# Optimization experiments

Hardware: AMD Instinct MI355X
Metric: run time of the kernel (lower is better)

Reference implementation:

```python
import jax, jax.numpy as jnp
import numpy as np

B, T, C = 4, 4096, 1024
DEGREE, EXPAND = 2, 2
H = EXPAND * C  # selector / inner dim = 2048


def setup_inputs() -> dict:
    key = jax.random.key(0)
    ks = jax.random.split(key, 4)
    sc = lambda d: 1.0 / np.sqrt(d)
    return {
        "x": jax.random.normal(ks[0], (B, T, C), jnp.float32),
        "W_sel": jax.random.normal(ks[1], (C, H), jnp.float32) * sc(C),
        "W_agg": jax.random.normal(ks[2], (C, DEGREE * H), jnp.float32) * sc(C),
        "W_out": jax.random.normal(ks[3], (H, C), jnp.float32) * sc(H),
        "sqk_q": jnp.ones((H,), jnp.float32),
        "sqk_k": jnp.ones((DEGREE * H,), jnp.float32),
    }


def reference(x, W_sel, W_agg, W_out, sqk_q, sqk_k):
    # Selector branch on queries (gated): B,T,H
    s = jax.nn.silu(jnp.einsum('btc,ch->bth', x, W_sel) * sqk_q)
    # Aggregator branch on context: B,T,DEGREE*H
    h = jnp.einsum('btc,cd->btd', x, W_agg) * sqk_k
    chunks = jnp.split(h, DEGREE, axis=-1)
    # Polynomial expansion: sum_{d=1..DEGREE} prod_{k<=d} chunk_k  -> B,T,H
    p = chunks[0]
    poly = p
    for c in chunks[1:]:
        p = p * c
        poly = poly + p
    # Causal masked mean: tril(ones(T,T)) @ poly / row-count == cumsum / arange.
    # Honors the causal structure without materializing the T x T mask.
    denom = jnp.arange(1, T + 1, dtype=poly.dtype)[None, :, None]
    agg = jnp.cumsum(poly, axis=1) / denom  # B,T,H causal running mean
    # Mix selected queries with aggregated polynomial state, project out.
    return jnp.einsum('bth,hc->btc', s * agg, W_out)
```

## Files before the change

### kernel.cpp

```cpp
#include <hip/hip_runtime.h>
#include <hip/hip_bf16.h>
#include <stdint.h>

#define BB 4
#define TT 4096
#define CC 1024
#define HH 2048
#define MM (BB*TT)
#define NCK 32
#define CKS 128

using short8 = __attribute__((ext_vector_type(8))) short;
using f32x4  = __attribute__((ext_vector_type(4))) float;

__device__ __forceinline__ unsigned short f2bf(float f) {
    union { float f; uint32_t u; } v; v.f = f;
    uint32_t r = v.u + 0x7fffu + ((v.u >> 16) & 1u);
    return (unsigned short)(r >> 16);
}
__device__ __forceinline__ float bf_lo(uint32_t u) {
    union { uint32_t u; float f; } v; v.u = u << 16; return v.f;
}
__device__ __forceinline__ float bf_hi(uint32_t u) {
    union { uint32_t u; float f; } v; v.u = u & 0xFFFF0000u; return v.f;
}
__device__ __forceinline__ uint32_t pack2bf(float lo, float hi) {
    return ((uint32_t)f2bf(lo)) | (((uint32_t)f2bf(hi)) << 16);
}

__global__ void conv_x_kernel(const float* __restrict__ x, unsigned short* __restrict__ xb, int n4) {
    int i = blockIdx.x * blockDim.x + threadIdx.x;
    if (i >= n4) return;
    float4 v = ((const float4*)x)[i];
    ushort4 o;
    o.x = f2bf(v.x); o.y = f2bf(v.y); o.z = f2bf(v.z); o.w = f2bf(v.w);
    ((ushort4*)xb)[i] = o;
}

__global__ void trans_direct_kernel(const float* __restrict__ in, unsigned short* __restrict__ out,
                                    const float* __restrict__ scale, int R, int Cin) {
    __shared__ float tile[32][33];
    int c0 = blockIdx.x * 32, k0 = blockIdx.y * 32;
    int tx = threadIdx.x;
    for (int i = threadIdx.y; i < 32; i += 8) {
        float s = scale ? scale[c0 + tx] : 1.f;
        tile[i][tx] = in[(size_t)(k0 + i) * Cin + c0 + tx] * s;
    }
    __syncthreads();
    for (int i = threadIdx.y; i < 32; i += 8)
        out[(size_t)(c0 + i) * R + k0 + tx] = f2bf(tile[tx][i]);
}

__global__ void trans_pair_kernel(const float* __restrict__ in, unsigned short* __restrict__ out,
                                  const float* __restrict__ scale) {
    __shared__ float tile[32][33];
    int q0 = blockIdx.x * 32, k0 = blockIdx.y * 32;
    int g = q0 >> 5;
    int tx = threadIdx.x;
    int c = (tx < 16) ? (g * 16 + tx) : (2048 + g * 16 + tx - 16);
    float s = scale[c];
    for (int i = threadIdx.y; i < 32; i += 8)
        tile[i][tx] = in[(size_t)(k0 + i) * 4096 + c] * s;
    __syncthreads();
    for (int i = threadIdx.y; i < 32; i += 8)
        out[(size_t)(q0 + i) * 1024 + k0 + tx] = f2bf(tile[tx][i]);
}

template<int LDK, int NT>
__device__ __forceinline__ void gemm_core(
    const unsigned short* __restrict__ A,
    const unsigned short* __restrict__ Bt,
    int m0, int n0, int tid,
    f32x4 (&acc)[8][4])
{
    __shared__ __align__(16) unsigned short As[4 * 8192];
    __shared__ __align__(16) unsigned short Bs[4 * 8192];

    const int lane = tid & 63;
    const int wave = tid >> 6;
    const int l15  = lane & 15;
    const int quad = lane >> 4;
    const int wm = (wave >> 2) << 7;
    const int wn = (wave & 3) << 6;

#pragma unroll
    for (int i = 0; i < 8; i++)
#pragma unroll
        for (int j = 0; j < 4; j++) acc[i][j] = {0.f, 0.f, 0.f, 0.f};

    const int rl  = tid >> 2;
    const int kc8 = ((tid & 3) ^ ((tid >> 3) & 3)) << 3;
    const unsigned short* gA = A  + (size_t)(m0 + rl) * LDK + kc8;
    const unsigned short* gB = Bt + (size_t)(n0 + rl) * LDK + kc8;

#define STAGE(G, L) __builtin_amdgcn_global_load_lds( \
        (const __attribute__((address_space(1))) void*)(G), \
        (__attribute__((address_space(3))) void*)(L), 16, 0, 0)

#pragma unroll
    for (int t = 0; t < 2; t++) {
        STAGE(gA + t * 32,             &As[t * 8192 + tid * 8]);
        STAGE(gA + 128 * LDK + t * 32, &As[t * 8192 + 4096 + tid * 8]);
        STAGE(gB + t * 32,             &Bs[t * 8192 + tid * 8]);
        STAGE(gB + 128 * LDK + t * 32, &Bs[t * 8192 + 4096 + tid * 8]);
    }
    asm volatile("s_waitcnt vmcnt(4)" ::: "memory");
    __builtin_amdgcn_s_barrier();

    for (int t = 0; t < NT; ++t) {
        const unsigned short* as = &As[(t & 3) * 8192];
        const unsigned short* bs = &Bs[(t & 3) * 8192];
        unsigned short* asd = &As[((t + 2) & 3) * 8192];
        unsigned short* bsd = &Bs[((t + 2) & 3) * 8192];
        const bool pf = (t + 2) < NT;

        short8 af[4], bf[4];
#pragma unroll
        for (int i = 0; i < 4; i++) {
            int row = wm + i * 16 + l15;
            af[i] = *(const short8*)(as + row * 32 + ((quad ^ ((row >> 1) & 3)) << 3));
        }
#pragma unroll
        for (int j = 0; j < 4; j++) {
            int row = wn + j * 16 + l15;
            bf[j] = *(const short8*)(bs + row * 32 + ((quad ^ ((row >> 1) & 3)) << 3));
        }
        if (pf) {
            STAGE(gA + (t + 2) * 32,             asd + tid * 8);
            STAGE(gA + 128 * LDK + (t + 2) * 32, asd + 4096 + tid * 8);
        }
        __builtin_amdgcn_s_barrier();
        asm volatile("s_waitcnt lgkmcnt(0)" ::: "memory");
        __builtin_amdgcn_sched_barrier(0);
        __builtin_amdgcn_s_setprio(1);
#pragma unroll
        for (int i = 0; i < 4; i++)
#pragma unroll
            for (int j = 0; j < 4; j++)
                acc[i][j] = __builtin_amdgcn_mfma_f32_16x16x32_bf16(af[i], bf[j], acc[i][j], 0, 0, 0);
        __builtin_amdgcn_s_setprio(0);
        __builtin_amdgcn_sched_barrier(0);
        __builtin_amdgcn_s_barrier();

        short8 ag[4];
#pragma unroll
        for (int i = 0; i < 4; i++) {
            int row = wm + 64 + i * 16 + l15;
            ag[i] = *(const short8*)(as + row * 32 + ((quad ^ ((row >> 1) & 3)) << 3));
        }
        if (pf) {
            STAGE(gB + (t + 2) * 32,             bsd + tid * 8);
            STAGE(gB + 128 * LDK + (t + 2) * 32, bsd + 4096 + tid * 8);
        }
        __builtin_amdgcn_s_barrier();
        asm volatile("s_waitcnt lgkmcnt(0)" ::: "memory");
        __builtin_amdgcn_sched_barrier(0);
        __builtin_amdgcn_s_setprio(1);
#pragma unroll
        for (int i = 0; i < 4; i++)
#pragma unroll
            for (int j = 0; j < 4; j++)
                acc[4 + i][j] = __builtin_amdgcn_mfma_f32_16x16x32_bf16(ag[i], bf[j], acc[4 + i][j], 0, 0, 0);
        __builtin_amdgcn_s_setprio(0);
        __builtin_amdgcn_sched_barrier(0);
        if (t < NT - 2) { asm volatile("s_waitcnt vmcnt(4)" ::: "memory"); }
        else            { asm volatile("s_waitcnt vmcnt(0)" ::: "memory"); }
        __builtin_amdgcn_s_barrier();
    }
#undef STAGE
}

__global__ __launch_bounds__(512, 2) void gemm_fused_kernel(
    const unsigned short* __restrict__ A,
    const unsigned short* __restrict__ Bt,
    unsigned short* __restrict__ Sout,
    unsigned short* __restrict__ Pout,
    float* __restrict__ part)
{
    __shared__ float psum[256];
    const int tid = threadIdx.x;
    const int mt = blockIdx.x / 24;
    const int nt = blockIdx.x % 24;
    const int m0 = mt << 8, n0 = nt << 8;
    if (tid < 256) psum[tid] = 0.f;

    f32x4 acc[8][4];
    gemm_core<1024, 32>(A, Bt, m0, n0, tid, acc);

    const int lane = tid & 63;
    const int wave = tid >> 6;
    const int l15  = lane & 15;
    const int quad = lane >> 4;
    const int wm = (wave >> 2) << 7;
    const int wn = (wave & 3) << 6;

    if (nt < 8) {
#pragma unroll
        for (int i = 0; i < 8; i++)
#pragma unroll
            for (int j = 0; j < 4; j++) {
                int col = n0 + wn + j * 16 + l15;
#pragma unroll
                for (int r = 0; r < 4; r++) {
                    int row = m0 + wm + i * 16 + quad * 4 + r;
                    float v = acc[i][j][r];
                    v = v / (1.f + __expf(-v));
                    Sout[(size_t)row * 2048 + col] = f2bf(v);
                }
            }
    } else {
        const int pbase = ((n0 - 2048 + wn) >> 1);
        float lsum0 = 0.f, lsum1 = 0.f;
#pragma unroll
        for (int i = 0; i < 8; i++) {
#pragma unroll
            for (int jp = 0; jp < 2; jp++) {
                int pcol = pbase + jp * 16 + l15;
#pragma unroll
                for (int r = 0; r < 4; r++) {
                    int row = m0 + wm + i * 16 + quad * 4 + r;
                    float pv = acc[i][2 * jp][r] * (1.f + acc[i][2 * jp + 1][r]);
                    Pout[(size_t)row * 2048 + pcol] = f2bf(pv);
                    if (jp == 0) lsum0 += pv; else lsum1 += pv;
                }
            }
        }
        int base = (wm >> 7) * 128 + (wn >> 1) + l15;
        atomicAdd(&psum[base], lsum0);
        atomicAdd(&psum[base + 16], lsum1);
        __syncthreads();
        if (tid < 256) {
            int b  = m0 >> 12;
            int ck = ((m0 & 4095) >> 7) + (tid >> 7);
            part[((size_t)b * NCK + ck) * 2048 + ((n0 - 2048) >> 1) + (tid & 127)] = psum[tid];
        }
    }
}

__global__ __launch_bounds__(512, 2) void gemm_out_kernel(
    const unsigned short* __restrict__ A,
    const unsigned short* __restrict__ Bt,
    float* __restrict__ Cout)
{
    const int tid = threadIdx.x;
    const int mt = blockIdx.x >> 2;
    const int nt = blockIdx.x & 3;
    const int m0 = mt << 8, n0 = nt << 8;

    f32x4 acc[8][4];
    gemm_core<2048, 64>(A, Bt, m0, n0, tid, acc);

    const int lane = tid & 63;
    const int wave = tid >> 6;
    const int l15  = lane & 15;
    const int quad = lane >> 4;
    const int wm = (wave >> 2) << 7;
    const int wn = (wave & 3) << 6;
#pragma unroll
    for (int i = 0; i < 8; i++)
#pragma unroll
        for (int j = 0; j < 4; j++) {
            int col = n0 + wn + j * 16 + l15;
#pragma unroll
            for (int r = 0; r < 4; r++) {
                int row = m0 + wm + i * 16 + quad * 4 + r;
                Cout[(size_t)row * 1024 + col] = acc[i][j][r];
            }
        }
}

__global__ void chunk_scan_kernel(float* __restrict__ part) {
    int idx = blockIdx.x * blockDim.x + threadIdx.x;
    int b = idx >> 11, col = idx & 2047;
    float run = 0.f;
    for (int ck = 0; ck < NCK; ck++) {
        size_t off = ((size_t)b * NCK + ck) * 2048 + col;
        float v = part[off];
        part[off] = run;
        run += v;
    }
}

__global__ void finalize_kernel(unsigned short* __restrict__ poly, const unsigned short* __restrict__ s,
                                const float* __restrict__ part) {
    int seg = blockIdx.x & 3;
    int ck  = (blockIdx.x >> 2) & (NCK - 1);
    int b   = blockIdx.x >> 7;
    int cp  = seg * 256 + threadIdx.x;
    size_t po = ((size_t)b * NCK + ck) * 2048 + cp * 2;
    float run0 = part[po], run1 = part[po + 1];
    size_t base = ((size_t)b * TT + (size_t)ck * CKS) * 2048 + cp * 2;
    for (int t = 0; t < CKS; t++) {
        int tg = ck * CKS + t;
        size_t off = base + (size_t)t * 2048;
        uint32_t pv = *(const uint32_t*)&poly[off];
        run0 += bf_lo(pv);
        run1 += bf_hi(pv);
        float inv = 1.f / (float)(tg + 1);
        uint32_t sv = *(const uint32_t*)&s[off];
        float m0 = bf_lo(sv) * run0 * inv;
        float m1 = bf_hi(sv) * run1 * inv;
        *(uint32_t*)&poly[off] = pack2bf(m0, m1);
    }
}

extern "C" void kernel_launch(void* const* d_in, const int* in_sizes, int n_in,
                              void* d_out, int out_size, void* d_ws, size_t ws_size,
                              hipStream_t stream) {
    const float* x     = (const float*)d_in[0];
    const float* W_sel = (const float*)d_in[1];
    const float* W_agg = (const float*)d_in[2];
    const float* W_out = (const float*)d_in[3];
    const float* sqk_q = (const float*)d_in[4];
    const float* sqk_k = (const float*)d_in[5];
    float* out = (float*)d_out;

    char* ws = (char*)d_ws;
    unsigned short* xb    = (unsigned short*)(ws);
    unsigned short* wallT = (unsigned short*)(ws + 33554432ull);
    unsigned short* woutT = (unsigned short*)(ws + 46137344ull);
    unsigned short* s_b   = (unsigned short*)(ws + 50331648ull);
    unsigned short* poly  = (unsigned short*)(ws + 117440512ull);
    float*          part  = (float*)(ws + 184549376ull);

    dim3 tb(32, 8);
    conv_x_kernel<<<(MM * CC / 4 + 255) / 256, 256, 0, stream>>>(x, xb, MM * CC / 4);
    trans_direct_kernel<<<dim3(HH / 32, CC / 32), tb, 0, stream>>>(W_sel, wallT, sqk_q, CC, HH);
    trans_pair_kernel<<<dim3(4096 / 32, CC / 32), tb, 0, stream>>>(W_agg, wallT + 2048ull * 1024, sqk_k);
    trans_direct_kernel<<<dim3(CC / 32, HH / 32), tb, 0, stream>>>(W_out, woutT, nullptr, HH, CC);

    gemm_fused_kernel<<<(MM / 256) * 24, 512, 0, stream>>>(xb, wallT, s_b, poly, part);

    chunk_scan_kernel<<<(BB * HH) / 256, 256, 0, stream>>>(part);
    finalize_kernel<<<BB * NCK * 4, 256, 0, stream>>>(poly, s_b, part);

    gemm_out_kernel<<<(MM / 256) * (CC / 256), 512, 0, stream>>>(poly, woutT, out);
}
```

Before: 473.0 us.

## Double-buffer LDS fragment loads and cut barriers per K-step in GEMM core

Restructures the GEMM main loop so the A/B register fragments for the next K-step are read from LDS while the current step's second MFMA half is still computing, using two register fragment buffers. The loop is unrolled by 4 over the LDS ring so buffer indices are compile-time constants. All four prefetch loads are issued at the start of each step, and the three barriers per step become one. The aim is to hide LDS read latency and remove barrier stalls, at the cost of more VGPRs under a 2-blocks-per-CU launch bound. Partial lgkmcnt waits also add ordering risk.

```diff
diff --git a/kernel.cpp b/kernel.cpp
--- a/kernel.cpp
+++ b/kernel.cpp
@@ -96,78 +96,94 @@
 #define STAGE(G, L) __builtin_amdgcn_global_load_lds( \
         (const __attribute__((address_space(1))) void*)(G), \
         (__attribute__((address_space(3))) void*)(L), 16, 0, 0)
+#define SWZ(row) ((quad ^ (((row) >> 1) & 3)) << 3)
 
 #pragma unroll
     for (int t = 0; t < 2; t++) {
         STAGE(gA + t * 32,             &As[t * 8192 + tid * 8]);
-        STAGE(gA + 128 * LDK + t * 32, &As[t * 8192 + 4096 + tid * 8]);
+        STAGE(gA + 128 * (size_t)LDK + t * 32, &As[t * 8192 + 4096 + tid * 8]);
         STAGE(gB + t * 32,             &Bs[t * 8192 + tid * 8]);
-        STAGE(gB + 128 * LDK + t * 32, &Bs[t * 8192 + 4096 + tid * 8]);
+        STAGE(gB + 128 * (size_t)LDK + t * 32, &Bs[t * 8192 + 4096 + tid * 8]);
     }
     asm volatile("s_waitcnt vmcnt(4)" ::: "memory");
     __builtin_amdgcn_s_barrier();
 
-    for (int t = 0; t < NT; ++t) {
-        const unsigned short* as = &As[(t & 3) * 8192];
-        const unsigned short* bs = &Bs[(t & 3) * 8192];
-        unsigned short* asd = &As[((t + 2) & 3) * 8192];
-        unsigned short* bsd = &Bs[((t + 2) & 3) * 8192];
-        const bool pf = (t + 2) < NT;
-
-        short8 af[4], bf[4];
-#pragma unroll
-        for (int i = 0; i < 4; i++) {
-            int row = wm + i * 16 + l15;
-            af[i] = *(const short8*)(as + row * 32 + ((quad ^ ((row >> 1) & 3)) << 3));
+    short8 afb[2][4], bfb[2][4], ag[4];
+#pragma unroll
+    for (int i = 0; i < 4; i++) {
+        int row = wm + i * 16 + l15;
+        afb[0][i] = *(const short8*)(&As[0] + row * 32 + SWZ(row));
+    }
+#pragma unroll
+    for (int j = 0; j < 4; j++) {
+        int row = wn + j * 16 + l15;
+        bfb[0][j] = *(const short8*)(&Bs[0] + row * 32 + SWZ(row));
+    }
+
+    for (int tb = 0; tb < NT; tb += 4) {
+#pragma unroll
+        for (int u = 0; u < 4; ++u) {
+            const int t   = tb + u;
+            const int cur = u & 1;
+            const int nxt = cur ^ 1;
+            const unsigned short* as  = &As[u * 8192];
+            const unsigned short* asn = &As[((u + 1) & 3) * 8192];
+            const unsigned short* bsn = &Bs[((u + 1) & 3) * 8192];
+            unsigned short* asd = &As[((u + 2) & 3) * 8192];
+            unsigned short* bsd = &Bs[((u + 2) & 3) * 8192];
+
+            if (t + 2 < NT) {
+                STAGE(gA + (size_t)(t + 2) * 32,                       asd + tid * 8);
+                STAGE(gA + 128 * (size_t)LDK + (size_t)(t + 2) * 32,   asd + 4096 + tid * 8);
+                STAGE(gB + (size_t)(t + 2) * 32,                       bsd + tid * 8);
+                STAGE(gB + 128 * (size_t)LDK + (size_t)(t + 2) * 32,   bsd + 4096 + tid * 8);
+            }
+#pragma unroll
+            for (int i = 0; i < 4; i++) {
+                int row = wm + 64 + i * 16 + l15;
+                ag[i] = *(const short8*)(as + row * 32 + SWZ(row));
+            }
+            asm volatile("s_waitcnt lgkmcnt(4)" ::: "memory");
+            __builtin_amdgcn_sched_barrier(0);
+            __builtin_amdgcn_s_setprio(1);
+#pragma unroll
+            for (int i = 0; i < 4; i++)
+#pragma unroll
+                for (int j = 0; j < 4; j++)
+                    acc[i][j] = __builtin_amdgcn_mfma_f32_16x16x32_bf16(afb[cur][i], bfb[cur][j], acc[i][j], 0, 0, 0);
+            __builtin_amdgcn_s_setprio(0);
+            __builtin_amdgcn_sched_barrier(0);
+            if (t < NT - 2) { asm volatile("s_waitcnt vmcnt(4)" ::: "memory"); }
+            else            { asm volatile("s_waitcnt vmcnt(0)" ::: "memory"); }
+            __builtin_amdgcn_s_barrier();
+            if (t + 1 < NT) {
+#pragma unroll
+                for (int i = 0; i < 4; i++) {
+                    int row = wm + i * 16 + l15;
+                    afb[nxt][i] = *(const short8*)(asn + row * 32 + SWZ(row));
+                }
+#pragma unroll
+                for (int j = 0; j < 4; j++) {
+                    int row = wn + j * 16 + l15;
+                    bfb[nxt][j] = *(const short8*)(bsn + row * 32 + SWZ(row));
+                }
+                asm volatile("s_waitcnt lgkmcnt(8)" ::: "memory");
+            } else {
+                asm volatile("s_waitcnt lgkmcnt(0)" ::: "memory");
+            }
+            __builtin_amdgcn_sched_barrier(0);
+            __builtin_amdgcn_s_setprio(1);
+#pragma unroll
+            for (int i = 0; i < 4; i++)
+#pragma unroll
+                for (int j = 0; j < 4; j++)
+                    acc[4 + i][j] = __builtin_amdgcn_mfma_f32_16x16x32_bf16(ag[i], bfb[cur][j], acc[4 + i][j], 0, 0, 0);
+            __builtin_amdgcn_s_setprio(0);
+            __builtin_amdgcn_sched_barrier(0);
         }
-#pragma unroll
-        for (int j = 0; j < 4; j++) {
-            int row = wn + j * 16 + l15;
-            bf[j] = *(const short8*)(bs + row * 32 + ((quad ^ ((row >> 1) & 3)) << 3));
-        }
-        if (pf) {
-            STAGE(gA + (t + 2) * 32,             asd + tid * 8);
-            STAGE(gA + 128 * LDK + (t + 2) * 32, asd + 4096 + tid * 8);
-        }
-        __builtin_amdgcn_s_barrier();
-        asm volatile("s_waitcnt lgkmcnt(0)" ::: "memory");
-        __builtin_amdgcn_sched_barrier(0);
-        __builtin_amdgcn_s_setprio(1);
-#pragma unroll
-        for (int i = 0; i < 4; i++)
-#pragma unroll
-            for (int j = 0; j < 4; j++)
-                acc[i][j] = __builtin_amdgcn_mfma_f32_16x16x32_bf16(af[i], bf[j], acc[i][j], 0, 0, 0);
-        __builtin_amdgcn_s_setprio(0);
-        __builtin_amdgcn_sched_barrier(0);
-        __builtin_amdgcn_s_barrier();
-
-        short8 ag[4];
-#pragma unroll
-        for (int i = 0; i < 4; i++) {
-            int row = wm + 64 + i * 16 + l15;
-            ag[i] = *(const short8*)(as + row * 32 + ((quad ^ ((row >> 1) & 3)) << 3));
-        }
-        if (pf) {
-            STAGE(gB + (t + 2) * 32,             bsd + tid * 8);
-            STAGE(gB + 128 * LDK + (t + 2) * 32, bsd + 4096 + tid * 8);
-        }
-        __builtin_amdgcn_s_barrier();
-        asm volatile("s_waitcnt lgkmcnt(0)" ::: "memory");
-        __builtin_amdgcn_sched_barrier(0);
-        __builtin_amdgcn_s_setprio(1);
-#pragma unroll
-        for (int i = 0; i < 4; i++)
-#pragma unroll
-            for (int j = 0; j < 4; j++)
-                acc[4 + i][j] = __builtin_amdgcn_mfma_f32_16x16x32_bf16(ag[i], bf[j], acc[4 + i][j], 0, 0, 0);
-        __builtin_amdgcn_s_setprio(0);
-        __builtin_amdgcn_sched_barrier(0);
-        if (t < NT - 2) { asm volatile("s_waitcnt vmcnt(4)" ::: "memory"); }
-        else            { asm volatile("s_waitcnt vmcnt(0)" ::: "memory"); }
-        __builtin_amdgcn_s_barrier();
     }
 #undef STAGE
+#undef SWZ
 }
 
 __global__ __launch_bounds__(512, 2) void gemm_fused_kernel(
```

New measurement: 590.5 us. 24.8% more time.

## Software-pipeline LDS fragment loads across k-tiles and drop the per-tile barrier

Applied to the files above, without the earlier changes.

Restructures the GEMM main loop so the next tile's A/B register fragments are read from LDS while the current tile's second MFMA half runs. Fragment sets are double-buffered and the loop is unrolled by 4, cutting the barriers per k-step from three to one. It also removes the min-blocks-per-CU of 2 from launch bounds, which lets the compiler use more registers for the extra fragment buffers, possibly at the cost of occupancy. The single barrier and partial lgkmcnt waits make correctness depend on the exact ordering of LDS reuse across the 4-stage ring.

```diff
diff --git a/kernel.cpp b/kernel.cpp
--- a/kernel.cpp
+++ b/kernel.cpp
@@ -96,81 +96,99 @@
 #define STAGE(G, L) __builtin_amdgcn_global_load_lds( \
         (const __attribute__((address_space(1))) void*)(G), \
         (__attribute__((address_space(3))) void*)(L), 16, 0, 0)
+#define SWZ(row) ((quad ^ (((row) >> 1) & 3)) << 3)
 
 #pragma unroll
     for (int t = 0; t < 2; t++) {
-        STAGE(gA + t * 32,             &As[t * 8192 + tid * 8]);
-        STAGE(gA + 128 * LDK + t * 32, &As[t * 8192 + 4096 + tid * 8]);
-        STAGE(gB + t * 32,             &Bs[t * 8192 + tid * 8]);
-        STAGE(gB + 128 * LDK + t * 32, &Bs[t * 8192 + 4096 + tid * 8]);
+        STAGE(gA + t * 32,                     &As[t * 8192 + tid * 8]);
+        STAGE(gA + 128 * (size_t)LDK + t * 32, &As[t * 8192 + 4096 + tid * 8]);
+        STAGE(gB + t * 32,                     &Bs[t * 8192 + tid * 8]);
+        STAGE(gB + 128 * (size_t)LDK + t * 32, &Bs[t * 8192 + 4096 + tid * 8]);
     }
     asm volatile("s_waitcnt vmcnt(4)" ::: "memory");
     __builtin_amdgcn_s_barrier();
 
-    for (int t = 0; t < NT; ++t) {
-        const unsigned short* as = &As[(t & 3) * 8192];
-        const unsigned short* bs = &Bs[(t & 3) * 8192];
-        unsigned short* asd = &As[((t + 2) & 3) * 8192];
-        unsigned short* bsd = &Bs[((t + 2) & 3) * 8192];
-        const bool pf = (t + 2) < NT;
-
-        short8 af[4], bf[4];
-#pragma unroll
-        for (int i = 0; i < 4; i++) {
-            int row = wm + i * 16 + l15;
-            af[i] = *(const short8*)(as + row * 32 + ((quad ^ ((row >> 1) & 3)) << 3));
-        }
-#pragma unroll
-        for (int j = 0; j < 4; j++) {
-            int row = wn + j * 16 + l15;
-            bf[j] = *(const short8*)(bs + row * 32 + ((quad ^ ((row >> 1) & 3)) << 3));
-        }
-        if (pf) {
-            STAGE(gA + (t + 2) * 32,             asd + tid * 8);
-            STAGE(gA + 128 * LDK + (t + 2) * 32, asd + 4096 + tid * 8);
-        }
-        __builtin_amdgcn_s_barrier();
-        asm volatile("s_waitcnt lgkmcnt(0)" ::: "memory");
-        __builtin_amdgcn_sched_barrier(0);
-        __builtin_amdgcn_s_setprio(1);
-#pragma unroll
-        for (int i = 0; i < 4; i++)
-#pragma unroll
-            for (int j = 0; j < 4; j++)
-                acc[i][j] = __builtin_amdgcn_mfma_f32_16x16x32_bf16(af[i], bf[j], acc[i][j], 0, 0, 0);
-        __builtin_amdgcn_s_setprio(0);
-        __builtin_amdgcn_sched_barrier(0);
-        __builtin_amdgcn_s_barrier();
-
-        short8 ag[4];
-#pragma unroll
-        for (int i = 0; i < 4; i++) {
-            int row = wm + 64 + i * 16 + l15;
-            ag[i] = *(const short8*)(as + row * 32 + ((quad ^ ((row >> 1) & 3)) << 3));
-        }
-        if (pf) {
-            STAGE(gB + (t + 2) * 32,             bsd + tid * 8);
-            STAGE(gB + 128 * LDK + (t + 2) * 32, bsd + 4096 + tid * 8);
-        }
-        __builtin_amdgcn_s_barrier();
-        asm volatile("s_waitcnt lgkmcnt(0)" ::: "memory");
-        __builtin_amdgcn_sched_barrier(0);
-        __builtin_amdgcn_s_setprio(1);
-#pragma unroll
-        for (int i = 0; i < 4; i++)
-#pragma unroll
-            for (int j = 0; j < 4; j++)
-                acc[4 + i][j] = __builtin_amdgcn_mfma_f32_16x16x32_bf16(ag[i], bf[j], acc[4 + i][j], 0, 0, 0);
-        __builtin_amdgcn_s_setprio(0);
-        __builtin_amdgcn_sched_barrier(0);
-        if (t < NT - 2) { asm volatile("s_waitcnt vmcnt(4)" ::: "memory"); }
-        else            { asm volatile("s_waitcnt vmcnt(0)" ::: "memory"); }
-        __builtin_amdgcn_s_barrier();
-    }
+    short8 af0[4], af1[4], bf0[4], bf1[4], ag[4];
+#pragma unroll
+    for (int i = 0; i < 4; i++) {
+        int row = wm + i * 16 + l15;
+        af0[i] = *(const short8*)(&As[0] + row * 32 + SWZ(row));
+    }
+#pragma unroll
+    for (int j = 0; j < 4; j++) {
+        int row = wn + j * 16 + l15;
+        bf0[j] = *(const short8*)(&Bs[0] + row * 32 + SWZ(row));
+    }
+
+#define TILE_BODY(U, AFC, AFN, BFC, BFN) { \
+    const int t = tb + (U); \
+    const unsigned short* as  = &As[(U) * 8192]; \
+    const unsigned short* asn = &As[(((U) + 1) & 3) * 8192]; \
+    const unsigned short* bsn = &Bs[(((U) + 1) & 3) * 8192]; \
+    unsigned short* asd = &As[(((U) + 2) & 3) * 8192]; \
+    unsigned short* bsd = &Bs[(((U) + 2) & 3) * 8192]; \
+    if (t + 2 < NT) { \
+        STAGE(gA + (size_t)(t + 2) * 32,                     asd + tid * 8); \
+        STAGE(gA + 128 * (size_t)LDK + (size_t)(t + 2) * 32, asd + 4096 + tid * 8); \
+        STAGE(gB + (size_t)(t + 2) * 32,                     bsd + tid * 8); \
+        STAGE(gB + 128 * (size_t)LDK + (size_t)(t + 2) * 32, bsd + 4096 + tid * 8); \
+    } \
+    _Pragma("unroll") \
+    for (int i = 0; i < 4; i++) { \
+        int row = wm + 64 + i * 16 + l15; \
+        ag[i] = *(const short8*)(as + row * 32 + SWZ(row)); \
+    } \
+    asm volatile("s_waitcnt lgkmcnt(4)" ::: "memory"); \
+    __builtin_amdgcn_sched_barrier(0); \
+    __builtin_amdgcn_s_setprio(1); \
+    _Pragma("unroll") \
+    for (int i = 0; i < 4; i++) \
+        _Pragma("unroll") \
+        for (int j = 0; j < 4; j++) \
+            acc[i][j] = __builtin_amdgcn_mfma_f32_16x16x32_bf16(AFC[i], BFC[j], acc[i][j], 0, 0, 0); \
+    __builtin_amdgcn_s_setprio(0); \
+    __builtin_amdgcn_sched_barrier(0); \
+    if (t < NT - 2) { asm volatile("s_waitcnt vmcnt(4)" ::: "memory"); } \
+    else            { asm volatile("s_waitcnt vmcnt(0)" ::: "memory"); } \
+    __builtin_amdgcn_s_barrier(); \
+    if (t + 1 < NT) { \
+        _Pragma("unroll") \
+        for (int i = 0; i < 4; i++) { \
+            int row = wm + i * 16 + l15; \
+            AFN[i] = *(const short8*)(asn + row * 32 + SWZ(row)); \
+        } \
+        _Pragma("unroll") \
+        for (int j = 0; j < 4; j++) { \
+            int row = wn + j * 16 + l15; \
+            BFN[j] = *(const short8*)(bsn + row * 32 + SWZ(row)); \
+        } \
+        asm volatile("s_waitcnt lgkmcnt(8)" ::: "memory"); \
+    } else { \
+        asm volatile("s_waitcnt lgkmcnt(0)" ::: "memory"); \
+    } \
+    __builtin_amdgcn_sched_barrier(0); \
+    __builtin_amdgcn_s_setprio(1); \
+    _Pragma("unroll") \
+    for (int i = 0; i < 4; i++) \
+        _Pragma("unroll") \
+        for (int j = 0; j < 4; j++) \
+            acc[4 + i][j] = __builtin_amdgcn_mfma_f32_16x16x32_bf16(ag[i], BFC[j], acc[4 + i][j], 0, 0, 0); \
+    __builtin_amdgcn_s_setprio(0); \
+    __builtin_amdgcn_sched_barrier(0); \
+}
+
+    for (int tb = 0; tb < NT; tb += 4) {
+        TILE_BODY(0, af0, af1, bf0, bf1)
+        TILE_BODY(1, af1, af0, bf1, bf0)
+        TILE_BODY(2, af0, af1, bf0, bf1)
+        TILE_BODY(3, af1, af0, bf1, bf0)
+    }
+#undef TILE_BODY
 #undef STAGE
-}
-
-__global__ __launch_bounds__(512, 2) void gemm_fused_kernel(
+#undef SWZ
+}
+
+__global__ __launch_bounds__(512) void gemm_fused_kernel(
     const unsigned short* __restrict__ A,
     const unsigned short* __restrict__ Bt,
     unsigned short* __restrict__ Sout,
@@ -237,7 +255,7 @@
     }
 }
 
-__global__ __launch_bounds__(512, 2) void gemm_out_kernel(
+__global__ __launch_bounds__(512) void gemm_out_kernel(
     const unsigned short* __restrict__ A,
     const unsigned short* __restrict__ Bt,
     float* __restrict__ Cout)
```

Result: slower. 584.9 us (+23.7%).
